# Performance work log

Hardware: AMD Instinct MI355X
Metric: run time of the kernel (lower is better)

Reference implementation:

```python
import jax, jax.numpy as jnp
import numpy as np

B = 16
N_F, D_F = 524288, 128  # total fine points, fine feature dim
N_C, D_C = 32768, 256   # total coarse points, coarse feature dim


def _ragged_lengths(total, n_seg, rng):
    # random positive lengths that sum exactly to `total`
    w = rng.uniform(0.5, 1.5, size=n_seg)
    l = np.floor(w / w.sum() * total).astype(np.int64)
    l[-1] += total - l.sum()
    return l


def setup_inputs() -> dict:
    key = jax.random.key(0)
    k1, k2 = jax.random.split(key)
    rng = np.random.default_rng(0)
    lengths_f = jnp.asarray(_ragged_lengths(N_F, B, rng))
    lengths_c = jnp.asarray(_ragged_lengths(N_C, B, rng))
    feats_f = jax.random.normal(k1, (N_F, D_F), dtype=jnp.float32)
    feats_c = jax.random.normal(k2, (N_C, D_C), dtype=jnp.float32)
    return {"feats_f": feats_f, "feats_c": feats_c,
            "lengths_f": lengths_f, "lengths_c": lengths_c}


def _segment_mean(feats, lengths, num_segments):
    # fused replacement for split_feats + pooling_feats:
    # segment id of row i = number of cumsum boundaries <= i
    n = feats.shape[0]
    seg = jnp.searchsorted(jnp.cumsum(lengths), jnp.arange(n), side='right')
    sums = jax.ops.segment_sum(feats, seg, num_segments=num_segments)  # [B, D]
    return sums / lengths[:, None].astype(feats.dtype)


def reference(feats_f, feats_c, lengths_f, lengths_c):
    global_feats_c = _segment_mean(feats_c, lengths_c, B)  # [B, D_C]
    global_feats_f = _segment_mean(feats_f, lengths_f, B)  # [B, D_F]
    return jnp.concatenate((global_feats_c, global_feats_f), axis=-1)  # [B, D_C+D_F]
```

## Files before the change

kernel.cpp:

```cpp
#include <hip/hip_runtime.h>

#define NSEG 16
#define OUT_COLS 384
#define OUT_ELEMS (NSEG * OUT_COLS)

__global__ __launch_bounds__(256) void seg_mean_kernel(
    const float4* __restrict__ ff, const float4* __restrict__ fc,
    const int* __restrict__ len_f, const int* __restrict__ len_c,
    float* __restrict__ outbuf, int fineBlocks, int iterF, int iterC, int nRep)
{
    __shared__ int   s_cum[NSEG];
    __shared__ float s_inv[NSEG];
    const bool fine = (int)blockIdx.x < fineBlocks;
    const int* len = fine ? len_f : len_c;
    if (threadIdx.x == 0) {
        int c = 0;
        for (int i = 0; i < NSEG; ++i) {
            int l = len[i];
            c += l;
            s_cum[i] = c;
            s_inv[i] = 1.0f / (float)l;
        }
    }
    __syncthreads();

    const int t = threadIdx.x;
    float* rep = outbuf + ((int)blockIdx.x % nRep) * OUT_ELEMS;

    int base, iters, colMask, rowShift, outOff;
    const float4* src;
    if (fine) {
        base = (int)blockIdx.x * 256 * iterF;
        iters = iterF; colMask = 31; rowShift = 5; outOff = 256; src = ff;
    } else {
        base = ((int)blockIdx.x - fineBlocks) * 256 * iterC;
        iters = iterC; colMask = 63; rowShift = 6; outOff = 0; src = fc;
    }
    const int col = (t & colMask) << 2;
    const int idx0 = base + t;

    int seg = 0;
    {
        int row = idx0 >> rowShift;
        while (row >= s_cum[seg]) ++seg;
    }
    int curEnd = s_cum[seg];
    float4 acc = make_float4(0.f, 0.f, 0.f, 0.f);

    int i = 0;
    for (;;) {
        int iCross = ((curEnd << rowShift) - idx0 + 255) >> 8;
        int spanEnd = iCross < iters ? iCross : iters;
        #pragma unroll 8
        for (; i < spanEnd; ++i) {
            const float4 v = src[idx0 + (i << 8)];
            acc.x += v.x; acc.y += v.y; acc.z += v.z; acc.w += v.w;
        }
        {
            const float inv = s_inv[seg];
            float* o = rep + seg * OUT_COLS + outOff + col;
            atomicAdd(o + 0, acc.x * inv);
            atomicAdd(o + 1, acc.y * inv);
            atomicAdd(o + 2, acc.z * inv);
            atomicAdd(o + 3, acc.w * inv);
        }
        if (i >= iters) break;
        acc = make_float4(0.f, 0.f, 0.f, 0.f);
        const int r = (idx0 + (i << 8)) >> rowShift;
        while (r >= s_cum[seg]) ++seg;
        curEnd = s_cum[seg];
    }
}

__global__ __launch_bounds__(256) void reduce_replicas_kernel(
    const float* __restrict__ ws, float* __restrict__ out, int nRep)
{
    const int j = blockIdx.x * blockDim.x + threadIdx.x;
    if (j < OUT_ELEMS) {
        float s = 0.f;
        for (int r = 0; r < nRep; ++r) s += ws[r * OUT_ELEMS + j];
        out[j] = s;
    }
}

extern "C" void kernel_launch(void* const* d_in, const int* in_sizes, int n_in,
                              void* d_out, int out_size, void* d_ws, size_t ws_size,
                              hipStream_t stream) {
    const float4* ff = (const float4*)d_in[0];
    const float4* fc = (const float4*)d_in[1];
    const int* lf = (const int*)d_in[2];
    const int* lc = (const int*)d_in[3];
    float* out = (float*)d_out;

    const int NF4 = in_sizes[0] / 4;
    const int NC4 = in_sizes[1] / 4;
    const int iterF = 32, iterC = 16;
    const int fineBlocks   = NF4 / (256 * iterF);
    const int coarseBlocks = NC4 / (256 * iterC);

    int nRep = (int)(ws_size / (OUT_ELEMS * sizeof(float)));
    if (nRep > 32) nRep = 32;
    if (nRep < 1)  nRep = 1;

    const size_t repBytes = (size_t)nRep * OUT_ELEMS * sizeof(float);
    hipMemsetAsync(d_ws, 0, repBytes, stream);

    seg_mean_kernel<<<fineBlocks + coarseBlocks, 256, 0, stream>>>(
        ff, fc, lf, lc, (float*)d_ws, fineBlocks, iterF, iterC, nRep);

    reduce_replicas_kernel<<<(OUT_ELEMS + 255) / 256, 256, 0, stream>>>(
        (const float*)d_ws, out, nRep);
}
```

Before: 412.0 us.

## Replace atomic replica accumulation with per-block partials and segment-aware reduce

Each block now accumulates into two register accumulators (current segment and next segment, assuming at most one boundary per block), reduces across threads in LDS, and writes a deterministic per-block partial slot instead of issuing global atomics into replicated buffers. The memset is removed, and a new reduce kernel sums the relevant block partials per segment and column. This removes atomic contention and the memset launch. The cost is an extra LDS reduction and barrier per block, and a reduce kernel that walks block ranges. It relies on each block spanning at most two segments.

```diff
diff --git a/kernel.cpp b/kernel.cpp
--- a/kernel.cpp
+++ b/kernel.cpp
@@ -2,15 +2,75 @@
 
 #define NSEG 16
 #define OUT_COLS 384
-#define OUT_ELEMS (NSEG * OUT_COLS)
+#define FINE_ITERS 32
+#define COARSE_ITERS 16
+
+
+template <int ITERS, int ROWSHIFT, int COLMASK, int DLOC>
+__device__ __forceinline__ void run_side(
+    const float4* __restrict__ src, int blockLocal,
+    const int* s_cum, const float* s_inv,
+    float* __restrict__ wsSlot,
+    float* __restrict__ lds)
+{
+    const int t = threadIdx.x;
+    const int idx0 = blockLocal * (256 * ITERS) + t;
+
+    const int firstRow = (blockLocal * (256 * ITERS)) >> ROWSHIFT;
+    int s0 = 0;
+    while (firstRow >= s_cum[s0]) ++s0;
+    const int bRow = s_cum[s0];
+
+    int iCross = ((bRow << ROWSHIFT) - idx0 + 255) >> 8;
+    if (iCross < 0) iCross = 0;
+    if (iCross > ITERS) iCross = ITERS;
+
+    float4 acc0 = make_float4(0.f, 0.f, 0.f, 0.f);
+    float4 acc1 = make_float4(0.f, 0.f, 0.f, 0.f);
+    #pragma unroll 16
+    for (int i = 0; i < ITERS; ++i) {
+        const float4 v = src[idx0 + (i << 8)];
+        const bool p = (i < iCross);
+        acc0.x += p ? v.x : 0.f;  acc1.x += p ? 0.f : v.x;
+        acc0.y += p ? v.y : 0.f;  acc1.y += p ? 0.f : v.y;
+        acc0.z += p ? v.z : 0.f;  acc1.z += p ? 0.f : v.z;
+        acc0.w += p ? v.w : 0.f;  acc1.w += p ? 0.f : v.w;
+    }
+
+    float4* l0 = (float4*)lds;
+    float4* l1 = (float4*)(lds + 1024);
+    l0[t] = acc0;
+    l1[t] = acc1;
+    __syncthreads();
+
+    if (t <= COLMASK) {
+        const float inv0 = s_inv[s0];
+        const float inv1 = s_inv[(s0 < NSEG - 1) ? s0 + 1 : s0];
+        float4 r0 = make_float4(0.f, 0.f, 0.f, 0.f);
+        float4 r1 = make_float4(0.f, 0.f, 0.f, 0.f);
+        #pragma unroll
+        for (int k = 0; k < 256 / (COLMASK + 1); ++k) {
+            const int tt = t + (COLMASK + 1) * k;
+            const float4 a = l0[tt];
+            const float4 b = l1[tt];
+            r0.x += a.x; r0.y += a.y; r0.z += a.z; r0.w += a.w;
+            r1.x += b.x; r1.y += b.y; r1.z += b.z; r1.w += b.w;
+        }
+        r0.x *= inv0; r0.y *= inv0; r0.z *= inv0; r0.w *= inv0;
+        r1.x *= inv1; r1.y *= inv1; r1.z *= inv1; r1.w *= inv1;
+        ((float4*)wsSlot)[t] = r0;
+        ((float4*)(wsSlot + DLOC))[t] = r1;
+    }
+}
 
 __global__ __launch_bounds__(256) void seg_mean_kernel(
     const float4* __restrict__ ff, const float4* __restrict__ fc,
     const int* __restrict__ len_f, const int* __restrict__ len_c,
-    float* __restrict__ outbuf, int fineBlocks, int iterF, int iterC, int nRep)
+    float* __restrict__ ws, int fineBlocks)
 {
     __shared__ int   s_cum[NSEG];
     __shared__ float s_inv[NSEG];
+    __shared__ float lds[2048];
     const bool fine = (int)blockIdx.x < fineBlocks;
     const int* len = fine ? len_f : len_c;
     if (threadIdx.x == 0) {
@@ -24,63 +84,55 @@
     }
     __syncthreads();
 
-    const int t = threadIdx.x;
-    float* rep = outbuf + ((int)blockIdx.x % nRep) * OUT_ELEMS;
-
-    int base, iters, colMask, rowShift, outOff;
-    const float4* src;
     if (fine) {
-        base = (int)blockIdx.x * 256 * iterF;
-        iters = iterF; colMask = 31; rowShift = 5; outOff = 256; src = ff;
+        const int b = (int)blockIdx.x;
+        run_side<FINE_ITERS, 5, 31, 128>(ff, b, s_cum, s_inv, ws + b * 256, lds);
     } else {
-        base = ((int)blockIdx.x - fineBlocks) * 256 * iterC;
-        iters = iterC; colMask = 63; rowShift = 6; outOff = 0; src = fc;
-    }
-    const int col = (t & colMask) << 2;
-    const int idx0 = base + t;
-
-    int seg = 0;
-    {
-        int row = idx0 >> rowShift;
-        while (row >= s_cum[seg]) ++seg;
-    }
-    int curEnd = s_cum[seg];
-    float4 acc = make_float4(0.f, 0.f, 0.f, 0.f);
-
-    int i = 0;
-    for (;;) {
-        int iCross = ((curEnd << rowShift) - idx0 + 255) >> 8;
-        int spanEnd = iCross < iters ? iCross : iters;
-        #pragma unroll 8
-        for (; i < spanEnd; ++i) {
-            const float4 v = src[idx0 + (i << 8)];
-            acc.x += v.x; acc.y += v.y; acc.z += v.z; acc.w += v.w;
-        }
-        {
-            const float inv = s_inv[seg];
-            float* o = rep + seg * OUT_COLS + outOff + col;
-            atomicAdd(o + 0, acc.x * inv);
-            atomicAdd(o + 1, acc.y * inv);
-            atomicAdd(o + 2, acc.z * inv);
-            atomicAdd(o + 3, acc.w * inv);
-        }
-        if (i >= iters) break;
-        acc = make_float4(0.f, 0.f, 0.f, 0.f);
-        const int r = (idx0 + (i << 8)) >> rowShift;
-        while (r >= s_cum[seg]) ++seg;
-        curEnd = s_cum[seg];
+        const int b = (int)blockIdx.x - fineBlocks;
+        run_side<COARSE_ITERS, 6, 63, 256>(fc, b, s_cum, s_inv,
+                                           ws + fineBlocks * 256 + b * 512, lds);
     }
 }
 
-__global__ __launch_bounds__(256) void reduce_replicas_kernel(
-    const float* __restrict__ ws, float* __restrict__ out, int nRep)
+__global__ __launch_bounds__(256) void reduce_kernel(
+    const float* __restrict__ ws,
+    const int* __restrict__ len_f, const int* __restrict__ len_c,
+    float* __restrict__ out, int fineBlocks, int coarseBlocks)
 {
-    const int j = blockIdx.x * blockDim.x + threadIdx.x;
-    if (j < OUT_ELEMS) {
-        float s = 0.f;
-        for (int r = 0; r < nRep; ++r) s += ws[r * OUT_ELEMS + j];
-        out[j] = s;
+    __shared__ int cum[NSEG];
+    const bool fine = (int)blockIdx.x < NSEG;
+    const int seg = (int)blockIdx.x & 15;
+    const int* len = fine ? len_f : len_c;
+    if (threadIdx.x == 0) {
+        int c = 0;
+        for (int i = 0; i < NSEG; ++i) { c += len[i]; cum[i] = c; }
     }
+    __syncthreads();
+
+    const int D = fine ? 128 : 256;
+    const int c = threadIdx.x;
+    if (c >= D) return;
+
+    const float* base = fine ? ws : ws + fineBlocks * 256;
+    const int shift = fine ? 8 : 6;
+    const int nb = fine ? fineBlocks : coarseBlocks;
+    const int slotSize = 2 * D;
+
+    const int cumM2 = (seg >= 2) ? cum[seg - 2] : 0;
+    int bStart = (cumM2 + (1 << shift) - 1) >> shift;
+    int bEnd = (cum[seg] - 1) >> shift;
+    if (bEnd > nb - 1) bEnd = nb - 1;
+
+    float acc = 0.f;
+    int s0 = 0;
+    for (int b = bStart; b <= bEnd; ++b) {
+        const int firstRow = b << shift;
+        while (firstRow >= cum[s0]) ++s0;
+        if (s0 > seg) break;
+        if (s0 == seg)          acc += base[b * slotSize + c];
+        else if (s0 + 1 == seg) acc += base[b * slotSize + D + c];
+    }
+    out[seg * OUT_COLS + (fine ? 256 + c : c)] = acc;
 }
 
 extern "C" void kernel_launch(void* const* d_in, const int* in_sizes, int n_in,
@@ -94,20 +146,12 @@
 
     const int NF4 = in_sizes[0] / 4;
     const int NC4 = in_sizes[1] / 4;
-    const int iterF = 32, iterC = 16;
-    const int fineBlocks   = NF4 / (256 * iterF);
-    const int coarseBlocks = NC4 / (256 * iterC);
-
-    int nRep = (int)(ws_size / (OUT_ELEMS * sizeof(float)));
-    if (nRep > 32) nRep = 32;
-    if (nRep < 1)  nRep = 1;
-
-    const size_t repBytes = (size_t)nRep * OUT_ELEMS * sizeof(float);
-    hipMemsetAsync(d_ws, 0, repBytes, stream);
+    const int fineBlocks   = NF4 / (256 * FINE_ITERS);
+    const int coarseBlocks = NC4 / (256 * COARSE_ITERS);
 
     seg_mean_kernel<<<fineBlocks + coarseBlocks, 256, 0, stream>>>(
-        ff, fc, lf, lc, (float*)d_ws, fineBlocks, iterF, iterC, nRep);
+        ff, fc, lf, lc, (float*)d_ws, fineBlocks);
 
-    reduce_replicas_kernel<<<(OUT_ELEMS + 255) / 256, 256, 0, stream>>>(
-        (const float*)d_ws, out, nRep);
+    reduce_kernel<<<2 * NSEG, 256, 0, stream>>>(
+        (const float*)d_ws, lf, lc, out, fineBlocks, coarseBlocks);
 }
```

Measured after the change: 502.4 us. 21.9% more time.
